# Performance work log

Hardware: AMD Instinct MI355X
Metric: run time of the kernel (lower is better)

The kernel has to match this reference:

```python
import jax, jax.numpy as jnp
import numpy as np

H, F, D, E, L = 8, 768, 128, 256, 13   # heads, feat_dim, compression_dim, embed_dim, nb_layer
B, T = 8, 1000
DCOR = D * (D - 1) // 2                # 8128, upper-triangle (offset=1) correlation features


def setup_inputs() -> dict:
    key = jax.random.key(0)
    ks = jax.random.split(key, 12)
    s = lambda k, shape, sc=0.02: jax.random.normal(k, shape, jnp.float32) * sc
    return {
        "x": jax.random.normal(ks[0], (B, F, T, L), jnp.float32),
        "weights_k": jnp.ones((H, L), jnp.float32),
        "weights_v": jnp.ones((H, L), jnp.float32),
        "q": jax.random.normal(ks[1], (H, D), jnp.float32),
        "Wk": s(ks[2], (H, D, F)), "bk": s(ks[3], (H, D)),
        "Wv": s(ks[4], (H, D, F)), "bv": s(ks[5], (H, D)),
        "Wproj": s(ks[6], (H, E, DCOR)), "bproj": s(ks[7], (H, E)),
        "WT": s(ks[8], (E, H * D)), "bT": s(ks[9], (E,)),
        "Wp": s(ks[10], (E, H * E)), "bp": s(ks[11], (E,)),
    }


def _norm_t(z):
    # normalize over the time axis; torch .var() is unbiased (ddof=1)
    mu = z.mean(axis=2, keepdims=True)
    sd = jnp.sqrt(z.var(axis=2, keepdims=True, ddof=1)) + 1e-9
    return (z - mu) / sd


def _forward(x, weights_k, weights_v, q, Wk, bk, Wv, bv, Wproj, bproj, WT, bT, Wp, bp):
    # x: [B, F, T, L]; per-head softmax-weighted layer sum -> [B, H, T, F]
    kw = jax.nn.softmax(weights_k, axis=-1)  # [H, L]
    vw = jax.nn.softmax(weights_v, axis=-1)
    k_raw = jnp.einsum('bftl,hl->bhtf', x, kw)
    v_raw = jnp.einsum('bftl,hl->bhtf', x, vw)
    # per-head compression linears -> [B, H, T, D]
    mh_k = jnp.einsum('bhtf,hdf->bhtd', k_raw, Wk) + bk[None, :, None, :]
    mh_v = jnp.einsum('bhtf,hdf->bhtd', v_raw, Wv) + bv[None, :, None, :]
    # single-query scaled-dot-product attention pooling per head
    scores = jnp.einsum('hd,bhtd->bht', q, mh_k) / jnp.sqrt(jnp.float32(D))
    attn = jax.nn.softmax(scores, axis=-1)
    o1 = jnp.einsum('bht,bhtd->bhd', attn, mh_v)           # [B, H, D]
    out_T = o1.reshape(B, H * D) @ WT.T + bT               # [B, E]
    # correlation branch (mh_q = mh_v): time-normalize, D x D correlation, triu(offset=1)
    k_n = _norm_t(mh_k)
    q_n = _norm_t(mh_v)
    corr = jnp.einsum('bhtk,bhtl->bhkl', k_n, q_n) / T     # [B, H, D, D]
    iu0, iu1 = np.triu_indices(D, k=1)
    mh_corr = corr[:, :, iu0, iu1]                         # [B, H, DCOR]
    outs = jnp.einsum('bhc,hec->bhe', mh_corr, Wproj) + bproj[None]
    out_F = outs.reshape(B, H * E) @ Wp.T + bp             # [B, E]
    return 0.5 * out_F + 0.5 * out_T


def reference(x, weights_k, weights_v, q, Wk, bk, Wv, bv, Wproj, bproj, WT, bT, Wp, bp):
    return _forward(x, weights_k, weights_v, q, Wk, bk, Wv, bv, Wproj, bproj, WT, bT, Wp, bp)
```

## Files before the change

### kernel.cpp

```cpp
#include <hip/hip_runtime.h>
#include <hip/hip_bf16.h>

#define Hn 8
#define Fn 768
#define Dn 128
#define En 256
#define Ln 13
#define Bn 8
#define Tn 1000
#define TPn 1024
#define NCOR 8128

typedef float f32x4 __attribute__((ext_vector_type(4)));
typedef __bf16 bf16x8 __attribute__((ext_vector_type(8)));
typedef unsigned short u16;

static __device__ __forceinline__ u16 f2bf(float f) {
  __hip_bfloat16 h = __float2bfloat16(f);
  return __builtin_bit_cast(u16, h);
}
static __device__ __forceinline__ float bf2f(u16 u) {
  return __bfloat162float(__builtin_bit_cast(__hip_bfloat16, u));
}

static __device__ __forceinline__ void gload_lds16(const u16* g, u16* lds_wave_base) {
  __builtin_amdgcn_global_load_lds(
      (const __attribute__((address_space(1))) unsigned int*)g,
      (__attribute__((address_space(3))) unsigned int*)lds_wave_base, 16, 0, 0);
}

__global__ __launch_bounds__(256) void k0_prep(
    const float* __restrict__ wk, const float* __restrict__ wv,
    const float* __restrict__ Wk, const float* __restrict__ Wv,
    float* __restrict__ kvw, u16* __restrict__ Wbf,
    float* __restrict__ s1, float* __restrict__ s2) {
  int gid = blockIdx.x * 256 + threadIdx.x;
  if (gid < 16) {
    int kv = gid >> 3, h = gid & 7;
    const float* w = (kv ? wv : wk) + h * Ln;
    float m = -1e30f;
    for (int l = 0; l < Ln; ++l) m = fmaxf(m, w[l]);
    float e[Ln], s = 0.f;
    for (int l = 0; l < Ln; ++l) { e[l] = expf(w[l] - m); s += e[l]; }
    for (int l = 0; l < Ln; ++l) kvw[(kv * Hn + h) * Ln + l] = e[l] / s;
  }
  int n = 2 * Hn * Dn * Fn;
  for (int i = gid; i < n; i += gridDim.x * 256) {
    float v = (i < Hn * Dn * Fn) ? Wk[i] : Wv[i - Hn * Dn * Fn];
    Wbf[i] = f2bf(v);
  }
  int ns = 2 * Bn * Hn * Dn;
  for (int i = gid; i < ns; i += gridDim.x * 256) { s1[i] = 0.f; s2[i] = 0.f; }
}

__global__ __launch_bounds__(256) void k1_raw(
    const float* __restrict__ x, const float* __restrict__ kvw_g,
    u16* __restrict__ kv_raw, int b0, int BG) {
  __shared__ float kvw[16 * Ln];
  __shared__ u16 res[16 * 32 * 34];
  int tid = threadIdx.x;
  if (tid < 16 * Ln) kvw[tid] = kvw_g[tid];
  int f0 = blockIdx.x * 32, t0 = blockIdx.y * 32;
  int b_l = blockIdx.z, b = b0 + b_l;
  int fl = tid & 31, tq = tid >> 5;
  int tbase = t0 + tq * 4;
  bool valid = (tbase < Tn);
  float4 xq[13];
  if (valid) {
    const float4* xp = (const float4*)(x + ((size_t)(b * Fn + f0 + fl) * Tn + tbase) * Ln);
#pragma unroll
    for (int i = 0; i < 13; ++i) xq[i] = xp[i];
  }
  __syncthreads();
  const float* xf = (const float*)xq;
  for (int o = 0; o < 16; ++o) {
    float a0 = 0.f, a1 = 0.f, a2 = 0.f, a3 = 0.f;
    if (valid) {
#pragma unroll
      for (int l = 0; l < Ln; ++l) {
        float w = kvw[o * Ln + l];
        a0 += xf[l] * w;
        a1 += xf[Ln + l] * w;
        a2 += xf[2 * Ln + l] * w;
        a3 += xf[3 * Ln + l] * w;
      }
    }
    int rb = o * 1088 + tq * 4 * 34 + fl;
    res[rb] = f2bf(a0);
    res[rb + 34] = f2bf(a1);
    res[rb + 68] = f2bf(a2);
    res[rb + 102] = f2bf(a3);
  }
  __syncthreads();
  int part = tid & 3;
#pragma unroll
  for (int it = 0; it < 8; ++it) {
    int r = (tid >> 2) + it * 64;
    int o = r >> 5, tl = r & 31;
    int kv = o >> 3, h = o & 7;
    const u16* src = res + o * 1088 + tl * 34 + part * 8;
    uint4 v;
    v.x = *(const unsigned*)(src + 0);
    v.y = *(const unsigned*)(src + 2);
    v.z = *(const unsigned*)(src + 4);
    v.w = *(const unsigned*)(src + 6);
    u16* dst = kv_raw + (((size_t)(kv * BG + b_l) * Hn + h) * TPn + t0 + tl) * Fn + f0 + part * 8;
    *reinterpret_cast<uint4*>(dst) = v;
  }
}

__global__ __launch_bounds__(256) void k2_gemm(
    const u16* __restrict__ kv_raw, const u16* __restrict__ Wbf,
    const float* __restrict__ bk, const float* __restrict__ bv,
    u16* __restrict__ mhT, float* __restrict__ s1buf, float* __restrict__ s2buf,
    int b0, int BG) {
  __shared__ __align__(16) char ldsbuf[128 * 130 * 2];
  u16* As = (u16*)ldsbuf;
  u16* Bs = (u16*)(ldsbuf + 8192);
  u16* Cst = (u16*)ldsbuf;
  int tid = threadIdx.x, lane = tid & 63, w = tid >> 6;
  int t0 = blockIdx.x * 128;
  int b_l = blockIdx.y / Hn, h = blockIdx.y % Hn, kv = blockIdx.z;
  int b = b0 + b_l;
  const u16* Abase = kv_raw + ((size_t)(kv * BG + b_l) * Hn + h) * TPn * Fn + (size_t)t0 * Fn;
  const u16* Bbase = Wbf + ((size_t)(kv * Hn + h)) * Dn * Fn;
  f32x4 acc[4][4];
#pragma unroll
  for (int mi = 0; mi < 4; ++mi)
#pragma unroll
    for (int ni = 0; ni < 4; ++ni) acc[mi][ni] = (f32x4){0.f, 0.f, 0.f, 0.f};
  int wm = (w >> 1) * 64, wn = (w & 1) * 64;
  int lin0 = tid, lin1 = tid + 256;
  int row0 = lin0 >> 2, part0 = lin0 & 3;
  int row1 = lin1 >> 2, part1 = lin1 & 3;
  int wb0 = (w * 64) * 8, wb1 = (256 + w * 64) * 8;
  for (int f0 = 0; f0 < Fn; f0 += 32) {
    __syncthreads();
    gload_lds16(Abase + (size_t)row0 * Fn + f0 + part0 * 8, As + wb0);
    gload_lds16(Abase + (size_t)row1 * Fn + f0 + part1 * 8, As + wb1);
    gload_lds16(Bbase + (size_t)row0 * Fn + f0 + part0 * 8, Bs + wb0);
    gload_lds16(Bbase + (size_t)row1 * Fn + f0 + part1 * 8, Bs + wb1);
    __syncthreads();
    bf16x8 af[4], bg[4];
#pragma unroll
    for (int mi = 0; mi < 4; ++mi)
      af[mi] = *(const bf16x8*)(As + (wm + mi * 16 + (lane & 15)) * 32 + (lane >> 4) * 8);
#pragma unroll
    for (int ni = 0; ni < 4; ++ni)
      bg[ni] = *(const bf16x8*)(Bs + (wn + ni * 16 + (lane & 15)) * 32 + (lane >> 4) * 8);
#pragma unroll
    for (int mi = 0; mi < 4; ++mi)
#pragma unroll
      for (int ni = 0; ni < 4; ++ni)
        acc[mi][ni] = __builtin_amdgcn_mfma_f32_16x16x32_bf16(af[mi], bg[ni], acc[mi][ni], 0, 0, 0);
  }
  float bias[4];
  const float* bptr = (kv ? bv : bk) + h * Dn;
#pragma unroll
  for (int ni = 0; ni < 4; ++ni) bias[ni] = bptr[wn + ni * 16 + (lane & 15)];
  __syncthreads();
#pragma unroll
  for (int mi = 0; mi < 4; ++mi)
#pragma unroll
    for (int ni = 0; ni < 4; ++ni)
#pragma unroll
      for (int r = 0; r < 4; ++r) {
        int row = wm + mi * 16 + (lane >> 4) * 4 + r;
        int col = wn + ni * 16 + (lane & 15);
        float v = acc[mi][ni][r] + bias[ni];
        if (t0 + row >= Tn) v = 0.f;
        Cst[row * 130 + col] = f2bf(v);
      }
  __syncthreads();
  int d = tid >> 1, half = tid & 1;
  u16* orow = mhT + (((size_t)(kv * Bn + b) * Hn + h) * Dn + d) * TPn + t0;
  float ssum = 0.f, ssq = 0.f;
#pragma unroll
  for (int j = 0; j < 8; ++j) {
    int tb = half * 64 + j * 8;
    u16 pk[8];
#pragma unroll
    for (int ii = 0; ii < 8; ++ii) {
      u16 ub = Cst[(tb + ii) * 130 + d];
      pk[ii] = ub;
      float vr = bf2f(ub);
      ssum += vr;
      ssq += vr * vr;
    }
    uint4 v4;
    v4.x = (unsigned)pk[0] | ((unsigned)pk[1] << 16);
    v4.y = (unsigned)pk[2] | ((unsigned)pk[3] << 16);
    v4.z = (unsigned)pk[4] | ((unsigned)pk[5] << 16);
    v4.w = (unsigned)pk[6] | ((unsigned)pk[7] << 16);
    *reinterpret_cast<uint4*>(orow + tb) = v4;
  }
  int sidx = ((kv * Bn + b) * Hn + h) * Dn + d;
  atomicAdd(&s1buf[sidx], ssum);
  atomicAdd(&s2buf[sidx], ssq);
}

__global__ __launch_bounds__(256) void k3_attn(
    const u16* __restrict__ mhT, const float* __restrict__ q, float* __restrict__ o1) {
  __shared__ float sc[TPn];
  __shared__ float qs[Dn];
  __shared__ float red[256];
  int tid = threadIdx.x;
  int b = blockIdx.x / Hn, h = blockIdx.x % Hn;
  const u16* K = mhT + ((size_t)(0 * Bn + b) * Hn + h) * Dn * TPn;
  const u16* V = mhT + ((size_t)(1 * Bn + b) * Hn + h) * Dn * TPn;
  if (tid < Dn) qs[tid] = q[h * Dn + tid];
  __syncthreads();
  const float scale = 0.088388347648318447f;
  int t4 = tid * 4;
  float s0 = 0.f, s1v = 0.f, s2v = 0.f, s3v = 0.f;
  for (int dd = 0; dd < Dn; ++dd) {
    ushort4 k4 = *(const ushort4*)(K + (size_t)dd * TPn + t4);
    float qv = qs[dd];
    s0 += qv * bf2f(k4.x);
    s1v += qv * bf2f(k4.y);
    s2v += qv * bf2f(k4.z);
    s3v += qv * bf2f(k4.w);
  }
  float z[4] = {s0 * scale, s1v * scale, s2v * scale, s3v * scale};
  float m = -1e30f;
#pragma unroll
  for (int j = 0; j < 4; ++j) {
    if (t4 + j >= Tn) z[j] = -1e30f;
    m = fmaxf(m, z[j]);
  }
  red[tid] = m;
  __syncthreads();
  for (int s = 128; s > 0; s >>= 1) { if (tid < s) red[tid] = fmaxf(red[tid], red[tid + s]); __syncthreads(); }
  m = red[0];
  __syncthreads();
  float lsum = 0.f;
#pragma unroll
  for (int j = 0; j < 4; ++j) {
    float e = (t4 + j < Tn) ? __expf(z[j] - m) : 0.f;
    sc[t4 + j] = e;
    lsum += e;
  }
  red[tid] = lsum;
  __syncthreads();
  for (int s = 128; s > 0; s >>= 1) { if (tid < s) red[tid] += red[tid + s]; __syncthreads(); }
  float inv = 1.f / red[0];
  __syncthreads();
  int d = tid >> 1, half = tid & 1;
  const u16* Vr = V + (size_t)d * TPn + half * 512;
  const float* at = sc + half * 512;
  float a = 0.f;
  for (int i = 0; i < 64; ++i) {
    bf16x8 vv = *(const bf16x8*)(Vr + i * 8);
#pragma unroll
    for (int j = 0; j < 8; ++j) a += at[i * 8 + j] * (float)vv[j];
  }
  red[tid] = a;
  __syncthreads();
  if (half == 0) o1[((size_t)b * Hn + h) * Dn + d] = inv * (red[tid] + red[tid + 1]);
}

__global__ __launch_bounds__(256) void k4_corr(
    const u16* __restrict__ mhT, const float* __restrict__ s1buf,
    const float* __restrict__ s2buf, float* __restrict__ corr) {
  __shared__ __align__(16) u16 As[128 * 32];
  __shared__ __align__(16) u16 Bs[128 * 32];
  __shared__ float mk[Dn], sk[Dn], mv[Dn], sv[Dn];
  int tid = threadIdx.x, lane = tid & 63, w = tid >> 6;
  int b = blockIdx.x / Hn, h = blockIdx.x % Hn;
  const u16* Kb = mhT + ((size_t)(0 * Bn + b) * Hn + h) * Dn * TPn;
  const u16* Vb = mhT + ((size_t)(1 * Bn + b) * Hn + h) * Dn * TPn;
  {
    int kv = tid >> 7, d = tid & 127;
    int sidx = ((kv * Bn + b) * Hn + h) * Dn + d;
    float a1 = s1buf[sidx], a2 = s2buf[sidx];
    float mu = a1 / (float)Tn;
    float var = (a2 - a1 * a1 / (float)Tn) / (float)(Tn - 1);
    float sd = sqrtf(fmaxf(var, 0.f)) + 1e-9f;
    if (kv == 0) { mk[d] = mu; sk[d] = sd; } else { mv[d] = mu; sv[d] = sd; }
  }
  f32x4 acc[4][4];
#pragma unroll
  for (int mi = 0; mi < 4; ++mi)
#pragma unroll
    for (int ni = 0; ni < 4; ++ni) acc[mi][ni] = (f32x4){0.f, 0.f, 0.f, 0.f};
  int wm = (w >> 1) * 64, wn = (w & 1) * 64;
  int lin0 = tid, lin1 = tid + 256;
  int row0 = lin0 >> 2, part0 = lin0 & 3;
  int row1 = lin1 >> 2, part1 = lin1 & 3;
  int wb0 = (w * 64) * 8, wb1 = (256 + w * 64) * 8;
  for (int t0 = 0; t0 < TPn; t0 += 32) {
    __syncthreads();
    gload_lds16(Kb + (size_t)row0 * TPn + t0 + part0 * 8, As + wb0);
    gload_lds16(Kb + (size_t)row1 * TPn + t0 + part1 * 8, As + wb1);
    gload_lds16(Vb + (size_t)row0 * TPn + t0 + part0 * 8, Bs + wb0);
    gload_lds16(Vb + (size_t)row1 * TPn + t0 + part1 * 8, Bs + wb1);
    __syncthreads();
    bf16x8 af[4], bg[4];
#pragma unroll
    for (int mi = 0; mi < 4; ++mi)
      af[mi] = *(const bf16x8*)(As + (wm + mi * 16 + (lane & 15)) * 32 + (lane >> 4) * 8);
#pragma unroll
    for (int ni = 0; ni < 4; ++ni)
      bg[ni] = *(const bf16x8*)(Bs + (wn + ni * 16 + (lane & 15)) * 32 + (lane >> 4) * 8);
#pragma unroll
    for (int mi = 0; mi < 4; ++mi)
#pragma unroll
      for (int ni = 0; ni < 4; ++ni)
        acc[mi][ni] = __builtin_amdgcn_mfma_f32_16x16x32_bf16(af[mi], bg[ni], acc[mi][ni], 0, 0, 0);
  }
  const float invT = 1.f / (float)Tn;
#pragma unroll
  for (int mi = 0; mi < 4; ++mi)
#pragma unroll
    for (int ni = 0; ni < 4; ++ni)
#pragma unroll
      for (int r = 0; r < 4; ++r) {
        int mm = wm + mi * 16 + (lane >> 4) * 4 + r;
        int nn = wn + ni * 16 + (lane & 15);
        if (nn > mm) {
          float S = acc[mi][ni][r];
          float cv = (S - (float)Tn * mk[mm] * mv[nn]) * invT / (sk[mm] * sv[nn]);
          int cidx = mm * (2 * Dn - mm - 1) / 2 + (nn - mm - 1);
          corr[((size_t)b * Hn + h) * NCOR + cidx] = cv;
        }
      }
}

__global__ __launch_bounds__(256) void k5_proj(
    const float* __restrict__ corr, const float* __restrict__ Wproj,
    const float* __restrict__ bproj, float* __restrict__ outs) {
  __shared__ float red[8 * 256];
  int tid = threadIdx.x;
  int e = blockIdx.x, h = blockIdx.y;
  const float4* wp4 = (const float4*)(Wproj + ((size_t)h * En + e) * NCOR);
  float accs[8];
#pragma unroll
  for (int b = 0; b < 8; ++b) accs[b] = 0.f;
  for (int k = 0; k < 8; ++k) {
    int c4 = tid + k * 256;
    if (c4 < NCOR / 4) {
      float4 wv = wp4[c4];
#pragma unroll
      for (int b = 0; b < 8; ++b) {
        float4 cv = *((const float4*)(corr + ((size_t)b * Hn + h) * NCOR) + c4);
        accs[b] += wv.x * cv.x + wv.y * cv.y + wv.z * cv.z + wv.w * cv.w;
      }
    }
  }
#pragma unroll
  for (int b = 0; b < 8; ++b) red[b * 256 + tid] = accs[b];
  __syncthreads();
  for (int s = 128; s > 0; s >>= 1) {
    if (tid < s) {
#pragma unroll
      for (int b = 0; b < 8; ++b) red[b * 256 + tid] += red[b * 256 + tid + s];
    }
    __syncthreads();
  }
  if (tid < 8) outs[((size_t)tid * Hn + h) * En + e] = red[tid * 256] + bproj[h * En + e];
}

__global__ __launch_bounds__(256) void k5_final(
    const float* __restrict__ outs, const float* __restrict__ o1,
    const float* __restrict__ WT, const float* __restrict__ bT,
    const float* __restrict__ Wp, const float* __restrict__ bp,
    float* __restrict__ out) {
  __shared__ float os[2048];
  __shared__ float o1s[1024];
  __shared__ float redF[256], redT[256];
  int tid = threadIdx.x;
  int b = blockIdx.x >> 3, ic = blockIdx.x & 7;
  for (int i = tid; i < 2048; i += 256) os[i] = outs[(size_t)b * 2048 + i];
  for (int i = tid; i < 1024; i += 256) o1s[i] = o1[(size_t)b * 1024 + i];
  __syncthreads();
  int il = tid >> 3, slice = tid & 7;
  int i = ic * 32 + il;
  const float* wpr = Wp + (size_t)i * 2048;
  const float* wtr = WT + (size_t)i * 1024;
  float aF = 0.f, aT = 0.f;
  for (int kk = 0; kk < 256; ++kk) { int j = kk * 8 + slice; aF += os[j] * wpr[j]; }
  for (int kk = 0; kk < 128; ++kk) { int j = kk * 8 + slice; aT += o1s[j] * wtr[j]; }
  redF[tid] = aF; redT[tid] = aT;
  __syncthreads();
  for (int s = 4; s > 0; s >>= 1) {
    if (slice < s) { redF[tid] += redF[tid + s]; redT[tid] += redT[tid + s]; }
    __syncthreads();
  }
  if (slice == 0) {
    float oF = redF[tid] + bp[i];
    float oT = redT[tid] + bT[i];
    out[(size_t)b * En + i] = 0.5f * oF + 0.5f * oT;
  }
}

extern "C" void kernel_launch(void* const* d_in, const int* in_sizes, int n_in,
                              void* d_out, int out_size, void* d_ws, size_t ws_size,
                              hipStream_t stream) {
  const float* x     = (const float*)d_in[0];
  const float* wk    = (const float*)d_in[1];
  const float* wv    = (const float*)d_in[2];
  const float* q     = (const float*)d_in[3];
  const float* Wk    = (const float*)d_in[4];
  const float* bk    = (const float*)d_in[5];
  const float* Wv    = (const float*)d_in[6];
  const float* bv    = (const float*)d_in[7];
  const float* Wproj = (const float*)d_in[8];
  const float* bproj = (const float*)d_in[9];
  const float* WT    = (const float*)d_in[10];
  const float* bT    = (const float*)d_in[11];
  const float* Wp    = (const float*)d_in[12];
  const float* bp    = (const float*)d_in[13];
  float* out = (float*)d_out;

  char* ws = (char*)d_ws;
  size_t off = 0;
  auto alloc = [&](size_t bytes) { size_t p = off; off += (bytes + 255) & ~(size_t)255; return p; };
  float* kvw  = (float*)(ws + alloc((size_t)2 * Hn * Ln * 4));
  u16*   Wbf  = (u16*)  (ws + alloc((size_t)2 * Hn * Dn * Fn * 2));
  u16*   mhT  = (u16*)  (ws + alloc((size_t)2 * Bn * Hn * Dn * TPn * 2));
  float* s1   = (float*)(ws + alloc((size_t)2 * Bn * Hn * Dn * 4));
  float* s2   = (float*)(ws + alloc((size_t)2 * Bn * Hn * Dn * 4));
  float* o1   = (float*)(ws + alloc((size_t)Bn * Hn * Dn * 4));
  float* corr = (float*)(ws + alloc((size_t)Bn * Hn * NCOR * 4));
  float* outs = (float*)(ws + alloc((size_t)Bn * Hn * En * 4));
  size_t fixed = off;
  size_t per_b = (size_t)2 * Hn * TPn * Fn * 2;
  int BG = 8;
  while (BG > 1 && fixed + (size_t)BG * per_b > ws_size) BG >>= 1;
  u16* kv_raw = (u16*)(ws + fixed);

  k0_prep<<<6144, 256, 0, stream>>>(wk, wv, Wk, Wv, kvw, Wbf, s1, s2);
  for (int b0 = 0; b0 < Bn; b0 += BG) {
    k1_raw<<<dim3(24, 32, BG), 256, 0, stream>>>(x, kvw, kv_raw, b0, BG);
    k2_gemm<<<dim3(8, Hn * BG, 2), 256, 0, stream>>>(kv_raw, Wbf, bk, bv, mhT, s1, s2, b0, BG);
  }
  k3_attn<<<64, 256, 0, stream>>>(mhT, q, o1);
  k4_corr<<<64, 256, 0, stream>>>(mhT, s1, s2, corr);
  k5_proj<<<dim3(En, Hn), 256, 0, stream>>>(corr, Wproj, bproj, outs);
  k5_final<<<64, 256, 0, stream>>>(outs, o1, WT, bT, Wp, bp, out);
}
```

Before: 702.3 us.

## Double-buffer GEMM staging, fuse attention scores into k2, split-T gram and PV kernels

Double-buffers the LDS tiles in the projection GEMM and the gram GEMM so global-to-LDS loads overlap the MFMA work. The attention scores are computed in the k2 epilogue from the staged K tile, which removes the separate scores pass over K. The PV step and the correlation gram are split across more blocks: four d-quarters for PV and four T-chunks for the gram, with partial gram sums written to a new workspace and reduced in a separate normalization kernel. This targets the low occupancy of the previous 64-block kernels, at the cost of an extra partial-sum buffer, more global traffic and one more launch.

```diff
diff --git a/kernel.cpp b/kernel.cpp
--- a/kernel.cpp
+++ b/kernel.cpp
@@ -112,16 +112,21 @@
 __global__ __launch_bounds__(256) void k2_gemm(
     const u16* __restrict__ kv_raw, const u16* __restrict__ Wbf,
     const float* __restrict__ bk, const float* __restrict__ bv,
+    const float* __restrict__ qg,
     u16* __restrict__ mhT, float* __restrict__ s1buf, float* __restrict__ s2buf,
-    int b0, int BG) {
-  __shared__ __align__(16) char ldsbuf[128 * 130 * 2];
-  u16* As = (u16*)ldsbuf;
-  u16* Bs = (u16*)(ldsbuf + 8192);
+    float* __restrict__ scores, int b0, int BG) {
+  __shared__ __align__(16) char ldsbuf[33280];
+  __shared__ float qsh[Dn];
+  u16* As0 = (u16*)ldsbuf;
+  u16* Bs0 = (u16*)(ldsbuf + 8192);
+  u16* As1 = (u16*)(ldsbuf + 16384);
+  u16* Bs1 = (u16*)(ldsbuf + 24576);
   u16* Cst = (u16*)ldsbuf;
   int tid = threadIdx.x, lane = tid & 63, w = tid >> 6;
   int t0 = blockIdx.x * 128;
   int b_l = blockIdx.y / Hn, h = blockIdx.y % Hn, kv = blockIdx.z;
   int b = b0 + b_l;
+  if (tid < Dn) qsh[tid] = qg[h * Dn + tid];
   const u16* Abase = kv_raw + ((size_t)(kv * BG + b_l) * Hn + h) * TPn * Fn + (size_t)t0 * Fn;
   const u16* Bbase = Wbf + ((size_t)(kv * Hn + h)) * Dn * Fn;
   f32x4 acc[4][4];
@@ -134,31 +139,43 @@
   int row0 = lin0 >> 2, part0 = lin0 & 3;
   int row1 = lin1 >> 2, part1 = lin1 & 3;
   int wb0 = (w * 64) * 8, wb1 = (256 + w * 64) * 8;
-  for (int f0 = 0; f0 < Fn; f0 += 32) {
-    __syncthreads();
-    gload_lds16(Abase + (size_t)row0 * Fn + f0 + part0 * 8, As + wb0);
-    gload_lds16(Abase + (size_t)row1 * Fn + f0 + part1 * 8, As + wb1);
-    gload_lds16(Bbase + (size_t)row0 * Fn + f0 + part0 * 8, Bs + wb0);
-    gload_lds16(Bbase + (size_t)row1 * Fn + f0 + part1 * 8, Bs + wb1);
-    __syncthreads();
+
+  auto STAGE = [&](int f0, u16* Ad, u16* Bd) {
+    gload_lds16(Abase + (size_t)row0 * Fn + f0 + part0 * 8, Ad + wb0);
+    gload_lds16(Abase + (size_t)row1 * Fn + f0 + part1 * 8, Ad + wb1);
+    gload_lds16(Bbase + (size_t)row0 * Fn + f0 + part0 * 8, Bd + wb0);
+    gload_lds16(Bbase + (size_t)row1 * Fn + f0 + part1 * 8, Bd + wb1);
+  };
+  auto COMPUTE = [&](const u16* Ac, const u16* Bc) {
     bf16x8 af[4], bg[4];
 #pragma unroll
     for (int mi = 0; mi < 4; ++mi)
-      af[mi] = *(const bf16x8*)(As + (wm + mi * 16 + (lane & 15)) * 32 + (lane >> 4) * 8);
+      af[mi] = *(const bf16x8*)(Ac + (wm + mi * 16 + (lane & 15)) * 32 + (lane >> 4) * 8);
 #pragma unroll
     for (int ni = 0; ni < 4; ++ni)
-      bg[ni] = *(const bf16x8*)(Bs + (wn + ni * 16 + (lane & 15)) * 32 + (lane >> 4) * 8);
+      bg[ni] = *(const bf16x8*)(Bc + (wn + ni * 16 + (lane & 15)) * 32 + (lane >> 4) * 8);
 #pragma unroll
     for (int mi = 0; mi < 4; ++mi)
 #pragma unroll
       for (int ni = 0; ni < 4; ++ni)
         acc[mi][ni] = __builtin_amdgcn_mfma_f32_16x16x32_bf16(af[mi], bg[ni], acc[mi][ni], 0, 0, 0);
-  }
+  };
+
+  STAGE(0, As0, Bs0);
+  __syncthreads();
+  for (int f0 = 0; f0 < Fn; f0 += 64) {
+    if (f0 + 32 < Fn) STAGE(f0 + 32, As1, Bs1);
+    COMPUTE(As0, Bs0);
+    __syncthreads();
+    if (f0 + 64 < Fn) STAGE(f0 + 64, As0, Bs0);
+    COMPUTE(As1, Bs1);
+    __syncthreads();
+  }
+
   float bias[4];
   const float* bptr = (kv ? bv : bk) + h * Dn;
 #pragma unroll
   for (int ni = 0; ni < 4; ++ni) bias[ni] = bptr[wn + ni * 16 + (lane & 15)];
-  __syncthreads();
 #pragma unroll
   for (int mi = 0; mi < 4; ++mi)
 #pragma unroll
@@ -197,37 +214,33 @@
   int sidx = ((kv * Bn + b) * Hn + h) * Dn + d;
   atomicAdd(&s1buf[sidx], ssum);
   atomicAdd(&s2buf[sidx], ssq);
-}
-
-__global__ __launch_bounds__(256) void k3_attn(
-    const u16* __restrict__ mhT, const float* __restrict__ q, float* __restrict__ o1) {
+
+  if (kv == 0) {
+    int t = tid >> 1, hf = tid & 1;
+    float s = 0.f;
+    const u16* crow = Cst + t * 130 + hf * 64;
+    const float* qh = qsh + hf * 64;
+#pragma unroll
+    for (int dd = 0; dd < 64; ++dd) s += qh[dd] * bf2f(crow[dd]);
+    s += __shfl_xor(s, 1);
+    if (hf == 0)
+      scores[((size_t)b * Hn + h) * TPn + t0 + t] =
+          (t0 + t < Tn) ? s * 0.088388347648318447f : -1e30f;
+  }
+}
+
+__global__ __launch_bounds__(256) void k3b_pv(
+    const u16* __restrict__ mhT, const float* __restrict__ scores,
+    float* __restrict__ o1) {
   __shared__ float sc[TPn];
-  __shared__ float qs[Dn];
   __shared__ float red[256];
   int tid = threadIdx.x;
-  int b = blockIdx.x / Hn, h = blockIdx.x % Hn;
-  const u16* K = mhT + ((size_t)(0 * Bn + b) * Hn + h) * Dn * TPn;
-  const u16* V = mhT + ((size_t)(1 * Bn + b) * Hn + h) * Dn * TPn;
-  if (tid < Dn) qs[tid] = q[h * Dn + tid];
-  __syncthreads();
-  const float scale = 0.088388347648318447f;
-  int t4 = tid * 4;
-  float s0 = 0.f, s1v = 0.f, s2v = 0.f, s3v = 0.f;
-  for (int dd = 0; dd < Dn; ++dd) {
-    ushort4 k4 = *(const ushort4*)(K + (size_t)dd * TPn + t4);
-    float qv = qs[dd];
-    s0 += qv * bf2f(k4.x);
-    s1v += qv * bf2f(k4.y);
-    s2v += qv * bf2f(k4.z);
-    s3v += qv * bf2f(k4.w);
-  }
-  float z[4] = {s0 * scale, s1v * scale, s2v * scale, s3v * scale};
-  float m = -1e30f;
-#pragma unroll
-  for (int j = 0; j < 4; ++j) {
-    if (t4 + j >= Tn) z[j] = -1e30f;
-    m = fmaxf(m, z[j]);
-  }
+  int bh = blockIdx.x >> 2, dq = blockIdx.x & 3;
+  int b = bh >> 3, h = bh & 7;
+  const float* srow = scores + (size_t)bh * TPn;
+  float4 z4 = *((const float4*)srow + tid);
+  float z[4] = {z4.x, z4.y, z4.z, z4.w};
+  float m = fmaxf(fmaxf(z[0], z[1]), fmaxf(z[2], z[3]));
   red[tid] = m;
   __syncthreads();
   for (int s = 128; s > 0; s >>= 1) { if (tid < s) red[tid] = fmaxf(red[tid], red[tid + s]); __syncthreads(); }
@@ -236,48 +249,40 @@
   float lsum = 0.f;
 #pragma unroll
   for (int j = 0; j < 4; ++j) {
-    float e = (t4 + j < Tn) ? __expf(z[j] - m) : 0.f;
-    sc[t4 + j] = e;
+    float e = __expf(z[j] - m);
+    sc[tid * 4 + j] = e;
     lsum += e;
   }
   red[tid] = lsum;
   __syncthreads();
   for (int s = 128; s > 0; s >>= 1) { if (tid < s) red[tid] += red[tid + s]; __syncthreads(); }
   float inv = 1.f / red[0];
-  __syncthreads();
-  int d = tid >> 1, half = tid & 1;
-  const u16* Vr = V + (size_t)d * TPn + half * 512;
-  const float* at = sc + half * 512;
+  int dl = tid & 31, slice = tid >> 5;
+  int d = dq * 32 + dl;
+  const u16* Vr = mhT + ((size_t)(1 * Bn + b) * Hn + h) * Dn * TPn + (size_t)d * TPn + slice * 128;
+  const float* at = sc + slice * 128;
   float a = 0.f;
-  for (int i = 0; i < 64; ++i) {
+#pragma unroll
+  for (int i = 0; i < 16; ++i) {
     bf16x8 vv = *(const bf16x8*)(Vr + i * 8);
 #pragma unroll
     for (int j = 0; j < 8; ++j) a += at[i * 8 + j] * (float)vv[j];
   }
+  __syncthreads();
   red[tid] = a;
   __syncthreads();
-  if (half == 0) o1[((size_t)b * Hn + h) * Dn + d] = inv * (red[tid] + red[tid + 1]);
-}
-
-__global__ __launch_bounds__(256) void k4_corr(
-    const u16* __restrict__ mhT, const float* __restrict__ s1buf,
-    const float* __restrict__ s2buf, float* __restrict__ corr) {
-  __shared__ __align__(16) u16 As[128 * 32];
-  __shared__ __align__(16) u16 Bs[128 * 32];
-  __shared__ float mk[Dn], sk[Dn], mv[Dn], sv[Dn];
+  for (int s = 128; s >= 32; s >>= 1) { if (tid < s) red[tid] += red[tid + s]; __syncthreads(); }
+  if (tid < 32) o1[((size_t)b * Hn + h) * Dn + dq * 32 + tid] = inv * red[tid];
+}
+
+__global__ __launch_bounds__(256) void k4a_gram(
+    const u16* __restrict__ mhT, float* __restrict__ Sgp) {
+  __shared__ __align__(16) u16 As0[4096], Bs0[4096], As1[4096], Bs1[4096];
   int tid = threadIdx.x, lane = tid & 63, w = tid >> 6;
-  int b = blockIdx.x / Hn, h = blockIdx.x % Hn;
+  int bh = blockIdx.x, tc = blockIdx.y;
+  int b = bh >> 3, h = bh & 7;
   const u16* Kb = mhT + ((size_t)(0 * Bn + b) * Hn + h) * Dn * TPn;
   const u16* Vb = mhT + ((size_t)(1 * Bn + b) * Hn + h) * Dn * TPn;
-  {
-    int kv = tid >> 7, d = tid & 127;
-    int sidx = ((kv * Bn + b) * Hn + h) * Dn + d;
-    float a1 = s1buf[sidx], a2 = s2buf[sidx];
-    float mu = a1 / (float)Tn;
-    float var = (a2 - a1 * a1 / (float)Tn) / (float)(Tn - 1);
-    float sd = sqrtf(fmaxf(var, 0.f)) + 1e-9f;
-    if (kv == 0) { mk[d] = mu; sk[d] = sd; } else { mv[d] = mu; sv[d] = sd; }
-  }
   f32x4 acc[4][4];
 #pragma unroll
   for (int mi = 0; mi < 4; ++mi)
@@ -288,27 +293,40 @@
   int row0 = lin0 >> 2, part0 = lin0 & 3;
   int row1 = lin1 >> 2, part1 = lin1 & 3;
   int wb0 = (w * 64) * 8, wb1 = (256 + w * 64) * 8;
-  for (int t0 = 0; t0 < TPn; t0 += 32) {
-    __syncthreads();
-    gload_lds16(Kb + (size_t)row0 * TPn + t0 + part0 * 8, As + wb0);
-    gload_lds16(Kb + (size_t)row1 * TPn + t0 + part1 * 8, As + wb1);
-    gload_lds16(Vb + (size_t)row0 * TPn + t0 + part0 * 8, Bs + wb0);
-    gload_lds16(Vb + (size_t)row1 * TPn + t0 + part1 * 8, Bs + wb1);
-    __syncthreads();
+  int tb = tc * 256;
+
+  auto STAGE = [&](int t0, u16* Ad, u16* Bd) {
+    gload_lds16(Kb + (size_t)row0 * TPn + t0 + part0 * 8, Ad + wb0);
+    gload_lds16(Kb + (size_t)row1 * TPn + t0 + part1 * 8, Ad + wb1);
+    gload_lds16(Vb + (size_t)row0 * TPn + t0 + part0 * 8, Bd + wb0);
+    gload_lds16(Vb + (size_t)row1 * TPn + t0 + part1 * 8, Bd + wb1);
+  };
+  auto COMPUTE = [&](const u16* Ac, const u16* Bc) {
     bf16x8 af[4], bg[4];
 #pragma unroll
     for (int mi = 0; mi < 4; ++mi)
-      af[mi] = *(const bf16x8*)(As + (wm + mi * 16 + (lane & 15)) * 32 + (lane >> 4) * 8);
+      af[mi] = *(const bf16x8*)(Ac + (wm + mi * 16 + (lane & 15)) * 32 + (lane >> 4) * 8);
 #pragma unroll
     for (int ni = 0; ni < 4; ++ni)
-      bg[ni] = *(const bf16x8*)(Bs + (wn + ni * 16 + (lane & 15)) * 32 + (lane >> 4) * 8);
+      bg[ni] = *(const bf16x8*)(Bc + (wn + ni * 16 + (lane & 15)) * 32 + (lane >> 4) * 8);
 #pragma unroll
     for (int mi = 0; mi < 4; ++mi)
 #pragma unroll
       for (int ni = 0; ni < 4; ++ni)
         acc[mi][ni] = __builtin_amdgcn_mfma_f32_16x16x32_bf16(af[mi], bg[ni], acc[mi][ni], 0, 0, 0);
-  }
-  const float invT = 1.f / (float)Tn;
+  };
+
+  STAGE(tb, As0, Bs0);
+  __syncthreads();
+  for (int s = 0; s < 256; s += 64) {
+    if (s + 32 < 256) STAGE(tb + s + 32, As1, Bs1);
+    COMPUTE(As0, Bs0);
+    __syncthreads();
+    if (s + 64 < 256) STAGE(tb + s + 64, As0, Bs0);
+    COMPUTE(As1, Bs1);
+    __syncthreads();
+  }
+  float* dst = Sgp + ((size_t)tc * 64 + bh) * 16384;
 #pragma unroll
   for (int mi = 0; mi < 4; ++mi)
 #pragma unroll
@@ -317,13 +335,50 @@
       for (int r = 0; r < 4; ++r) {
         int mm = wm + mi * 16 + (lane >> 4) * 4 + r;
         int nn = wn + ni * 16 + (lane & 15);
-        if (nn > mm) {
-          float S = acc[mi][ni][r];
-          float cv = (S - (float)Tn * mk[mm] * mv[nn]) * invT / (sk[mm] * sv[nn]);
-          int cidx = mm * (2 * Dn - mm - 1) / 2 + (nn - mm - 1);
-          corr[((size_t)b * Hn + h) * NCOR + cidx] = cv;
-        }
+        dst[mm * 128 + nn] = acc[mi][ni][r];
       }
+}
+
+__global__ __launch_bounds__(256) void k4b_corr(
+    const float* __restrict__ Sgp, const float* __restrict__ s1buf,
+    const float* __restrict__ s2buf, float* __restrict__ corr) {
+  __shared__ float mkS[32], skS[32], mvS[128], svS[128];
+  int tid = threadIdx.x;
+  int bh = blockIdx.x >> 2, quad = blockIdx.x & 3;
+  int b = bh >> 3, h = bh & 7;
+  if (tid < 32) {
+    int dd = quad * 32 + tid;
+    int sidx = ((0 * Bn + b) * Hn + h) * Dn + dd;
+    float a1 = s1buf[sidx], a2 = s2buf[sidx];
+    float mu = a1 / (float)Tn;
+    float var = (a2 - a1 * a1 / (float)Tn) / (float)(Tn - 1);
+    mkS[tid] = mu;
+    skS[tid] = sqrtf(fmaxf(var, 0.f)) + 1e-9f;
+  } else if (tid < 160) {
+    int dd = tid - 32;
+    int sidx = ((1 * Bn + b) * Hn + h) * Dn + dd;
+    float a1 = s1buf[sidx], a2 = s2buf[sidx];
+    float mu = a1 / (float)Tn;
+    float var = (a2 - a1 * a1 / (float)Tn) / (float)(Tn - 1);
+    mvS[dd] = mu;
+    svS[dd] = sqrtf(fmaxf(var, 0.f)) + 1e-9f;
+  }
+  __syncthreads();
+  const float invT = 1.f / (float)Tn;
+#pragma unroll
+  for (int it = 0; it < 16; ++it) {
+    int cell = it * 256 + tid;
+    int ml = cell >> 7, nn = cell & 127;
+    int mm = quad * 32 + ml;
+    if (nn > mm) {
+      size_t off = (size_t)bh * 16384 + mm * 128 + nn;
+      float S = Sgp[off] + Sgp[off + (size_t)64 * 16384] +
+                Sgp[off + (size_t)128 * 16384] + Sgp[off + (size_t)192 * 16384];
+      float cv = (S - (float)Tn * mkS[ml] * mvS[nn]) * invT / (skS[ml] * svS[nn]);
+      int cidx = mm * (2 * Dn - mm - 1) / 2 + (nn - mm - 1);
+      corr[(size_t)bh * NCOR + cidx] = cv;
+    }
+  }
 }
 
 __global__ __launch_bounds__(256) void k5_proj(
@@ -415,14 +470,16 @@
   char* ws = (char*)d_ws;
   size_t off = 0;
   auto alloc = [&](size_t bytes) { size_t p = off; off += (bytes + 255) & ~(size_t)255; return p; };
-  float* kvw  = (float*)(ws + alloc((size_t)2 * Hn * Ln * 4));
-  u16*   Wbf  = (u16*)  (ws + alloc((size_t)2 * Hn * Dn * Fn * 2));
-  u16*   mhT  = (u16*)  (ws + alloc((size_t)2 * Bn * Hn * Dn * TPn * 2));
-  float* s1   = (float*)(ws + alloc((size_t)2 * Bn * Hn * Dn * 4));
-  float* s2   = (float*)(ws + alloc((size_t)2 * Bn * Hn * Dn * 4));
-  float* o1   = (float*)(ws + alloc((size_t)Bn * Hn * Dn * 4));
-  float* corr = (float*)(ws + alloc((size_t)Bn * Hn * NCOR * 4));
-  float* outs = (float*)(ws + alloc((size_t)Bn * Hn * En * 4));
+  float* kvw    = (float*)(ws + alloc((size_t)2 * Hn * Ln * 4));
+  u16*   Wbf    = (u16*)  (ws + alloc((size_t)2 * Hn * Dn * Fn * 2));
+  u16*   mhT    = (u16*)  (ws + alloc((size_t)2 * Bn * Hn * Dn * TPn * 2));
+  float* s1     = (float*)(ws + alloc((size_t)2 * Bn * Hn * Dn * 4));
+  float* s2     = (float*)(ws + alloc((size_t)2 * Bn * Hn * Dn * 4));
+  float* o1     = (float*)(ws + alloc((size_t)Bn * Hn * Dn * 4));
+  float* corr   = (float*)(ws + alloc((size_t)Bn * Hn * NCOR * 4));
+  float* outs   = (float*)(ws + alloc((size_t)Bn * Hn * En * 4));
+  float* scores = (float*)(ws + alloc((size_t)Bn * Hn * TPn * 4));
+  float* Sgp    = (float*)(ws + alloc((size_t)4 * Bn * Hn * Dn * Dn * 4));
   size_t fixed = off;
   size_t per_b = (size_t)2 * Hn * TPn * Fn * 2;
   int BG = 8;
@@ -432,10 +489,12 @@
   k0_prep<<<6144, 256, 0, stream>>>(wk, wv, Wk, Wv, kvw, Wbf, s1, s2);
   for (int b0 = 0; b0 < Bn; b0 += BG) {
     k1_raw<<<dim3(24, 32, BG), 256, 0, stream>>>(x, kvw, kv_raw, b0, BG);
-    k2_gemm<<<dim3(8, Hn * BG, 2), 256, 0, stream>>>(kv_raw, Wbf, bk, bv, mhT, s1, s2, b0, BG);
-  }
-  k3_attn<<<64, 256, 0, stream>>>(mhT, q, o1);
-  k4_corr<<<64, 256, 0, stream>>>(mhT, s1, s2, corr);
+    k2_gemm<<<dim3(8, Hn * BG, 2), 256, 0, stream>>>(kv_raw, Wbf, bk, bv, q, mhT, s1, s2,
+                                                     scores, b0, BG);
+  }
+  k3b_pv<<<256, 256, 0, stream>>>(mhT, scores, o1);
+  k4a_gram<<<dim3(64, 4), 256, 0, stream>>>(mhT, Sgp);
+  k4b_corr<<<256, 256, 0, stream>>>(Sgp, s1, s2, corr);
   k5_proj<<<dim3(En, Hn), 256, 0, stream>>>(corr, Wproj, bproj, outs);
   k5_final<<<64, 256, 0, stream>>>(outs, o1, WT, bT, Wp, bp, out);
 }
```

Result: faster. 681.1 us (-3.0%).
